# Optimization experiments

Measured on AMD Instinct MI355X. Metric: run time of the kernel, lower is better.

Reference implementation:

```python
import jax, jax.numpy as jnp
import numpy as np

T, B, IN = 64, 4096, 145
H1, H2 = 150, 32


def _lstm_layer(x, w_ih, w_hh, b_ih, b_hh):
    """Single LSTM layer, PyTorch gate order (i, f, g, o).
    x: (T, B, in_dim); w_ih: (4H, in_dim); w_hh: (4H, H); biases: (4H,).
    Returns hidden sequence (T, B, H)."""
    H = w_hh.shape[1]
    Bsz = x.shape[1]
    # Precompute input contribution for all timesteps at once (one big GEMM).
    xg = jnp.einsum('tbi,gi->tbg', x, w_ih) + (b_ih + b_hh)  # (T, B, 4H)
    w_hh_t = w_hh.T  # (H, 4H)

    def step(carry, xg_t):
        h, c = carry
        gates = xg_t + h @ w_hh_t  # (B, 4H)
        i, f, g, o = jnp.split(gates, 4, axis=-1)
        i = jax.nn.sigmoid(i)
        f = jax.nn.sigmoid(f)
        g = jnp.tanh(g)
        o = jax.nn.sigmoid(o)
        c = f * c + i * g
        h = o * jnp.tanh(c)
        return (h, c), h

    h0 = jnp.zeros((Bsz, H), x.dtype)
    c0 = jnp.zeros((Bsz, H), x.dtype)
    _, hs = jax.lax.scan(step, (h0, c0), xg)
    return hs  # (T, B, H)


def _init_lstm_params(key, in_dim, hidden):
    # PyTorch init: U(-k, k) with k = 1/sqrt(hidden)
    k = 1.0 / np.sqrt(hidden)
    ks = jax.random.split(key, 4)
    w_ih = jax.random.uniform(ks[0], (4 * hidden, in_dim), jnp.float32, -k, k)
    w_hh = jax.random.uniform(ks[1], (4 * hidden, hidden), jnp.float32, -k, k)
    b_ih = jax.random.uniform(ks[2], (4 * hidden,), jnp.float32, -k, k)
    b_hh = jax.random.uniform(ks[3], (4 * hidden,), jnp.float32, -k, k)
    return w_ih, w_hh, b_ih, b_hh


def setup_inputs() -> dict:
    key = jax.random.key(0)
    kx, k0, k1, k2 = jax.random.split(key, 4)
    x = jax.random.normal(kx, (T, B, IN), jnp.float32)
    w_ih_l0, w_hh_l0, b_ih_l0, b_hh_l0 = _init_lstm_params(k0, IN, H1)
    w_ih_l1, w_hh_l1, b_ih_l1, b_hh_l1 = _init_lstm_params(k1, H1, H1)
    w_ih_l2, w_hh_l2, b_ih_l2, b_hh_l2 = _init_lstm_params(k2, H1, H2)
    return {
        'x': x,
        'w_ih_l0': w_ih_l0, 'w_hh_l0': w_hh_l0, 'b_ih_l0': b_ih_l0, 'b_hh_l0': b_hh_l0,
        'w_ih_l1': w_ih_l1, 'w_hh_l1': w_hh_l1, 'b_ih_l1': b_ih_l1, 'b_hh_l1': b_hh_l1,
        'w_ih_l2': w_ih_l2, 'w_hh_l2': w_hh_l2, 'b_ih_l2': b_ih_l2, 'b_hh_l2': b_hh_l2,
    }


def reference(x,
              w_ih_l0, w_hh_l0, b_ih_l0, b_hh_l0,
              w_ih_l1, w_hh_l1, b_ih_l1, b_hh_l1,
              w_ih_l2, w_hh_l2, b_ih_l2, b_hh_l2):
    # temporal_model1: 2-layer LSTM (145 -> 150 -> 150)
    h = _lstm_layer(x, w_ih_l0, w_hh_l0, b_ih_l0, b_hh_l0)
    h = _lstm_layer(h, w_ih_l1, w_hh_l1, b_ih_l1, b_hh_l1)
    # temporal_model2: 1-layer LSTM (150 -> 32)
    out2 = _lstm_layer(h, w_ih_l2, w_hh_l2, b_ih_l2, b_hh_l2)
    return out2  # (T, B, 32)
```

## Files before the change

### kernel.cpp

```cpp
#include <hip/hip_runtime.h>


typedef _Float16 f16;
typedef _Float16 f16x8 __attribute__((ext_vector_type(8)));
typedef _Float16 f16x4 __attribute__((ext_vector_type(4)));
typedef float f32x4 __attribute__((ext_vector_type(4)));

#define T_STEPS 64
#define BATCH 4096

__device__ __forceinline__ float fexp(float x) {
  return __builtin_amdgcn_exp2f(x * 1.44269504088896340736f);
}
__device__ __forceinline__ float sigf(float x) {
  return __builtin_amdgcn_rcpf(1.0f + fexp(-x));
}
__device__ __forceinline__ float tanh_f(float x) {
  return 1.0f - 2.0f * __builtin_amdgcn_rcpf(1.0f + fexp(2.0f * x));
}

#define BAR_LGKM() asm volatile("s_waitcnt lgkmcnt(0)\n\ts_barrier" ::: "memory")

__global__ __launch_bounds__(256) void prep_w(
    const float* __restrict__ wih0, const float* __restrict__ bih0, const float* __restrict__ bhh0,
    const float* __restrict__ wih1, const float* __restrict__ bih1, const float* __restrict__ bhh1,
    f16* __restrict__ wprep0, f16* __restrict__ wprep1,
    float* __restrict__ bias0, float* __restrict__ bias1) {
  int idx = blockIdx.x * 256 + threadIdx.x;
  constexpr int WE = 640 * 168;
  if (idx < WE) {
    int c = idx / 168, k = idx - c * 168;
    int gate = c / 160, cg = c - gate * 160;
    float v = (cg < 150 && k < 145) ? wih0[(size_t)(gate * 150 + cg) * 145 + k] : 0.f;
    wprep0[idx] = (f16)v;
  } else if (idx < 2 * WE) {
    int e = idx - WE;
    int c = e / 168, k = e - c * 168;
    int gate = c / 160, cg = c - gate * 160;
    float v = (cg < 150 && k < 150) ? wih1[(size_t)(gate * 150 + cg) * 150 + k] : 0.f;
    wprep1[e] = (f16)v;
  } else if (idx < 2 * WE + 640) {
    int c = idx - 2 * WE;
    int gate = c / 160, cg = c - gate * 160;
    bias0[c] = (cg < 150) ? (bih0[gate * 150 + cg] + bhh0[gate * 150 + cg]) : 0.f;
  } else if (idx < 2 * WE + 1280) {
    int c = idx - 2 * WE - 640;
    int gate = c / 160, cg = c - gate * 160;
    bias1[c] = (cg < 150) ? (bih1[gate * 150 + cg] + bhh1[gate * 150 + cg]) : 0.f;
  }
}

template <int IN_DIM, int SRC_F16>
__global__ __launch_bounds__(512, 4) void gemm_xg4(
    const float* __restrict__ xin_f32, const f16* __restrict__ xin_f16,
    const f16* __restrict__ wprep, const float* __restrict__ bias_pre,
    f16* __restrict__ xg) {
  constexpr int ASTR = 168;
  __shared__ __align__(16) f16 A_lds[128 * ASTR];
  __shared__ __align__(16) f16 W_lds[64 * ASTR];
  __shared__ __align__(16) float bias_lds[640];
  const int tid = threadIdx.x;
  const int mtile = blockIdx.x;
  const int g0 = mtile * 128;

  if constexpr (SRC_F16) {
#pragma unroll
    for (int q = 0; q < 6; ++q) {
      int i = q * 512 + tid;
      if (i < 2688)
        *(f16x8*)(&A_lds[i * 8]) = *(const f16x8*)(xin_f16 + (size_t)g0 * ASTR + (size_t)i * 8);
    }
  } else {
#pragma unroll
    for (int q = 0; q < 10; ++q) {
      int idx = q * 512 + tid;
      int r = idx / 40, c4 = (idx - r * 40) * 4;
      f16x4 o;
      if (c4 + 4 <= IN_DIM) {
        f32x4 v;
        __builtin_memcpy(&v, xin_f32 + (size_t)(g0 + r) * IN_DIM + c4, 16);
#pragma unroll
        for (int j = 0; j < 4; ++j) o[j] = (f16)v[j];
      } else {
#pragma unroll
        for (int j = 0; j < 4; ++j)
          o[j] = (c4 + j < IN_DIM) ? (f16)xin_f32[(size_t)(g0 + r) * IN_DIM + c4 + j] : (f16)0.f;
      }
      *(f16x4*)(&A_lds[r * ASTR + c4]) = o;
    }
  }
  if (tid < 160) *(f32x4*)(&bias_lds[tid * 4]) = *(const f32x4*)(bias_pre + tid * 4);
#pragma unroll
  for (int q = 0; q < 3; ++q) {
    int i = q * 512 + tid;
    if (i < 1344) *(f16x8*)(&W_lds[i * 8]) = *(const f16x8*)(wprep + (size_t)i * 8);
  }
  BAR_LGKM();

  const int l = tid & 63, wv = tid >> 6;
  const int p = wv >> 1, cq = wv & 1;
  const int lrow = l & 15, lk8 = (l >> 4) * 8, r0 = (l >> 4) * 4;
  const int arow0 = (2 * p) * 16 + lrow;
  const int wrow0 = (2 * cq) * 16 + lrow;

  f16x8 pv0, pv1, pv2;
  for (int ch = 0; ch < 10; ++ch) {
    if (ch < 9) {
      const f16* wsrc = wprep + (size_t)(ch + 1) * 10752;
      pv0 = *(const f16x8*)(wsrc + (size_t)tid * 8);
      pv1 = *(const f16x8*)(wsrc + (size_t)(tid + 512) * 8);
      if (tid < 320) pv2 = *(const f16x8*)(wsrc + (size_t)(tid + 1024) * 8);
    }
    const int c0 = ch * 64 + (2 * cq) * 16 + lrow;
    const float bs0 = bias_lds[c0], bs1 = bias_lds[c0 + 16];
    f32x4 a00 = {bs0, bs0, bs0, bs0}, a01 = {bs1, bs1, bs1, bs1};
    f32x4 a10 = a00, a11 = a01;
#pragma unroll
    for (int kc = 0; kc < 5; ++kc) {
      f16x8 a0 = *(const f16x8*)(&A_lds[arow0 * ASTR + kc * 32 + lk8]);
      f16x8 a1 = *(const f16x8*)(&A_lds[(arow0 + 16) * ASTR + kc * 32 + lk8]);
      f16x8 b0 = *(const f16x8*)(&W_lds[wrow0 * ASTR + kc * 32 + lk8]);
      f16x8 b1 = *(const f16x8*)(&W_lds[(wrow0 + 16) * ASTR + kc * 32 + lk8]);
      a00 = __builtin_amdgcn_mfma_f32_16x16x32_f16(a0, b0, a00, 0, 0, 0);
      a01 = __builtin_amdgcn_mfma_f32_16x16x32_f16(a0, b1, a01, 0, 0, 0);
      a10 = __builtin_amdgcn_mfma_f32_16x16x32_f16(a1, b0, a10, 0, 0, 0);
      a11 = __builtin_amdgcn_mfma_f32_16x16x32_f16(a1, b1, a11, 0, 0, 0);
    }
    {
      f16x4 o;
      size_t rg0 = (size_t)(mtile * 8 + 2 * p);
#pragma unroll
      for (int j = 0; j < 4; ++j) o[j] = (f16)a00[j];
      *(f16x4*)(xg + (rg0 * 640 + c0) * 16 + r0) = o;
#pragma unroll
      for (int j = 0; j < 4; ++j) o[j] = (f16)a01[j];
      *(f16x4*)(xg + (rg0 * 640 + c0 + 16) * 16 + r0) = o;
#pragma unroll
      for (int j = 0; j < 4; ++j) o[j] = (f16)a10[j];
      *(f16x4*)(xg + ((rg0 + 1) * 640 + c0) * 16 + r0) = o;
#pragma unroll
      for (int j = 0; j < 4; ++j) o[j] = (f16)a11[j];
      *(f16x4*)(xg + ((rg0 + 1) * 640 + c0 + 16) * 16 + r0) = o;
    }
    if (ch < 9) {
      BAR_LGKM();
      *(f16x8*)(&W_lds[tid * 8]) = pv0;
      *(f16x8*)(&W_lds[(tid + 512) * 8]) = pv1;
      if (tid < 320) *(f16x8*)(&W_lds[(tid + 1024) * 8]) = pv2;
      BAR_LGKM();
    }
  }
}

__global__ __launch_bounds__(640, 2) void lstm_rec(
    const f16* __restrict__ xg, const float* __restrict__ whh,
    f16* __restrict__ hout) {
  constexpr int H = 150, HSTR = 168, CPAD = 640;
  __shared__ __align__(16) f16 hbuf[2][16 * HSTR];
  const int tid = threadIdx.x;
  const int l = tid & 63, w = tid >> 6;
  const int lrow = l & 15, lk8 = (l >> 4) * 8, r0 = (l >> 4) * 4;
  const int col = w * 16 + lrow;
  const int bx = blockIdx.x, b0 = bx * 16;

  for (int i = tid; i < 2 * 16 * HSTR / 8; i += 640) {
    f16x8 z = {};
    *(f16x8*)(&hbuf[0][0] + (size_t)i * 8) = z;
  }

  f16x8 wh[4][5];
#pragma unroll
  for (int g = 0; g < 4; ++g)
#pragma unroll
    for (int kc = 0; kc < 5; ++kc) {
      f16x8 v;
#pragma unroll
      for (int j = 0; j < 8; ++j) {
        int k = kc * 32 + lk8 + j;
        float x = (col < H && k < H) ? whh[((size_t)g * H + col) * H + k] : 0.f;
        v[j] = (f16)x;
      }
      wh[g][kc] = v;
    }
  __syncthreads();

  float creg[4] = {0.f, 0.f, 0.f, 0.f};
  f16x4 pv[4];
#pragma unroll
  for (int g = 0; g < 4; ++g)
    pv[g] = *(const f16x4*)(xg + ((size_t)bx * CPAD + g * 160 + col) * 16 + r0);

  for (int t = 0; t < T_STEPS; ++t) {
    const int cur = t & 1, nxt = cur ^ 1;

    f32x4 acc[4];
#pragma unroll
    for (int g = 0; g < 4; ++g) {
#pragma unroll
      for (int j = 0; j < 4; ++j) acc[g][j] = (float)pv[g][j];
    }
    if (t + 1 < T_STEPS) {
#pragma unroll
      for (int g = 0; g < 4; ++g)
        pv[g] = *(const f16x4*)(xg + ((size_t)((t + 1) * 256 + bx) * CPAD + g * 160 + col) * 16 + r0);
    }
    if (t > 0 && tid < 336) {
      f16x8 v = *(const f16x8*)(&hbuf[cur][tid * 8]);
      *(f16x8*)(hout + ((size_t)(t - 1) * BATCH + b0) * 168 + (size_t)tid * 8) = v;
    }

#pragma unroll
    for (int kc = 0; kc < 5; ++kc) {
      f16x8 a = *(const f16x8*)(&hbuf[cur][lrow * HSTR + kc * 32 + lk8]);
#pragma unroll
      for (int g = 0; g < 4; ++g)
        acc[g] = __builtin_amdgcn_mfma_f32_16x16x32_f16(a, wh[g][kc], acc[g], 0, 0, 0);
    }

#pragma unroll
    for (int j = 0; j < 4; ++j) {
      float iv = sigf(acc[0][j]);
      float fv = sigf(acc[1][j]);
      float gv = tanh_f(acc[2][j]);
      float ov = sigf(acc[3][j]);
      float c = fv * creg[j] + iv * gv;
      creg[j] = c;
      float h = ov * tanh_f(c);
      hbuf[nxt][(r0 + j) * HSTR + col] = (f16)h;
    }

    BAR_LGKM();
  }
  if (tid < 336) {
    f16x8 v = *(const f16x8*)(&hbuf[0][tid * 8]);
    *(f16x8*)(hout + ((size_t)(T_STEPS - 1) * BATCH + b0) * 168 + (size_t)tid * 8) = v;
  }
}

__global__ __launch_bounds__(640, 2) void lstm_rec1f(
    const f16* __restrict__ xg, const float* __restrict__ whh,
    const float* __restrict__ wih2, const float* __restrict__ bih2,
    const float* __restrict__ bhh2, f16* __restrict__ xg2) {
  constexpr int H = 150, HSTR = 168, CPAD = 640;
  __shared__ __align__(16) f16 hbuf[2][16 * HSTR];
  const int tid = threadIdx.x;
  const int l = tid & 63, w = tid >> 6;
  const int lrow = l & 15, lk8 = (l >> 4) * 8, r0 = (l >> 4) * 4;
  const int col = w * 16 + lrow;
  const int bx = blockIdx.x;
  const bool xw = (w < 8);
  const int c2 = w * 16 + lrow;

  for (int i = tid; i < 2 * 16 * HSTR / 8; i += 640) {
    f16x8 z = {};
    *(f16x8*)(&hbuf[0][0] + (size_t)i * 8) = z;
  }

  f16x8 wh[4][5];
#pragma unroll
  for (int g = 0; g < 4; ++g)
#pragma unroll
    for (int kc = 0; kc < 5; ++kc) {
      f16x8 v;
#pragma unroll
      for (int j = 0; j < 8; ++j) {
        int k = kc * 32 + lk8 + j;
        float x = (col < H && k < H) ? whh[((size_t)g * H + col) * H + k] : 0.f;
        v[j] = (f16)x;
      }
      wh[g][kc] = v;
    }
  f16x8 wx2[5];
  float bias2 = 0.f;
  if (xw) {
#pragma unroll
    for (int kc = 0; kc < 5; ++kc) {
      f16x8 v;
#pragma unroll
      for (int j = 0; j < 8; ++j) {
        int k = kc * 32 + lk8 + j;
        float x = (k < 150) ? wih2[(size_t)c2 * 150 + k] : 0.f;
        v[j] = (f16)x;
      }
      wx2[kc] = v;
    }
    bias2 = bih2[c2] + bhh2[c2];
  }
  __syncthreads();

  float creg[4] = {0.f, 0.f, 0.f, 0.f};
  f16x4 pv[4];
#pragma unroll
  for (int g = 0; g < 4; ++g)
    pv[g] = *(const f16x4*)(xg + ((size_t)bx * CPAD + g * 160 + col) * 16 + r0);

  for (int t = 0; t < T_STEPS; ++t) {
    const int cur = t & 1, nxt = cur ^ 1;

    f32x4 acc[4];
#pragma unroll
    for (int g = 0; g < 4; ++g) {
#pragma unroll
      for (int j = 0; j < 4; ++j) acc[g][j] = (float)pv[g][j];
    }
    if (t + 1 < T_STEPS) {
#pragma unroll
      for (int g = 0; g < 4; ++g)
        pv[g] = *(const f16x4*)(xg + ((size_t)((t + 1) * 256 + bx) * CPAD + g * 160 + col) * 16 + r0);
    }

    f32x4 accx = {bias2, bias2, bias2, bias2};
#pragma unroll
    for (int kc = 0; kc < 5; ++kc) {
      f16x8 a = *(const f16x8*)(&hbuf[cur][lrow * HSTR + kc * 32 + lk8]);
#pragma unroll
      for (int g = 0; g < 4; ++g)
        acc[g] = __builtin_amdgcn_mfma_f32_16x16x32_f16(a, wh[g][kc], acc[g], 0, 0, 0);
      if (xw)
        accx = __builtin_amdgcn_mfma_f32_16x16x32_f16(a, wx2[kc], accx, 0, 0, 0);
    }
    if (xw && t > 0) {
      f16x4 o;
#pragma unroll
      for (int j = 0; j < 4; ++j) o[j] = (f16)accx[j];
      *(f16x4*)(xg2 + (((size_t)(t - 1) * 256 + bx) * 128 + c2) * 16 + r0) = o;
    }

#pragma unroll
    for (int j = 0; j < 4; ++j) {
      float iv = sigf(acc[0][j]);
      float fv = sigf(acc[1][j]);
      float gv = tanh_f(acc[2][j]);
      float ov = sigf(acc[3][j]);
      float c = fv * creg[j] + iv * gv;
      creg[j] = c;
      float h = ov * tanh_f(c);
      hbuf[nxt][(r0 + j) * HSTR + col] = (f16)h;
    }

    BAR_LGKM();
  }
  if (xw) {
    f32x4 accx = {bias2, bias2, bias2, bias2};
#pragma unroll
    for (int kc = 0; kc < 5; ++kc) {
      f16x8 a = *(const f16x8*)(&hbuf[0][lrow * HSTR + kc * 32 + lk8]);
      accx = __builtin_amdgcn_mfma_f32_16x16x32_f16(a, wx2[kc], accx, 0, 0, 0);
    }
    f16x4 o;
#pragma unroll
    for (int j = 0; j < 4; ++j) o[j] = (f16)accx[j];
    *(f16x4*)(xg2 + (((size_t)(T_STEPS - 1) * 256 + bx) * 128 + c2) * 16 + r0) = o;
  }
}

__global__ __launch_bounds__(128) void lstm_rec32(
    const f16* __restrict__ xg2, const float* __restrict__ whh2,
    float* __restrict__ yout) {
  constexpr int HSTR2 = 40;
  __shared__ __align__(16) f16 hbuf2[2][16 * HSTR2];
  const int tid = threadIdx.x;
  const int l = tid & 63, w = tid >> 6;
  const int lrow = l & 15, lk8 = (l >> 4) * 8, r0 = (l >> 4) * 4;
  const int cg = w * 16 + lrow;
  const int p = blockIdx.x;
  const int rg = p >> 1, half = p & 1;
  const int b0 = p * 8;
  const bool active = (l < 32);

  for (int i = tid; i < 2 * 16 * HSTR2 / 8; i += 128) {
    f16x8 z = {};
    *(f16x8*)(&hbuf2[0][0] + (size_t)i * 8) = z;
  }

  f16x8 wh2[4];
#pragma unroll
  for (int g = 0; g < 4; ++g) {
    f16x8 v;
#pragma unroll
    for (int j = 0; j < 8; ++j)
      v[j] = (f16)whh2[(size_t)(g * 32 + cg) * 32 + lk8 + j];
    wh2[g] = v;
  }
  __syncthreads();

  float creg[4] = {0.f, 0.f, 0.f, 0.f};
  f16x4 pv[4];
  if (active) {
#pragma unroll
    for (int g = 0; g < 4; ++g)
      pv[g] = *(const f16x4*)(xg2 + ((size_t)rg * 128 + g * 32 + cg) * 16 + half * 8 + r0);
  }

  for (int t = 0; t < T_STEPS; ++t) {
    const int cur = t & 1, nxt = cur ^ 1;

    f32x4 acc[4];
    if (active) {
#pragma unroll
      for (int g = 0; g < 4; ++g) {
#pragma unroll
        for (int j = 0; j < 4; ++j) acc[g][j] = (float)pv[g][j];
      }
      if (t + 1 < T_STEPS) {
#pragma unroll
        for (int g = 0; g < 4; ++g)
          pv[g] = *(const f16x4*)(xg2 + (((size_t)(t + 1) * 256 + rg) * 128 + g * 32 + cg) * 16 + half * 8 + r0);
      }
    } else {
#pragma unroll
      for (int g = 0; g < 4; ++g) acc[g] = f32x4{0.f, 0.f, 0.f, 0.f};
    }

    {
      f16x8 a = *(const f16x8*)(&hbuf2[cur][lrow * HSTR2 + lk8]);
#pragma unroll
      for (int g = 0; g < 4; ++g)
        acc[g] = __builtin_amdgcn_mfma_f32_16x16x32_f16(a, wh2[g], acc[g], 0, 0, 0);
    }

    if (active) {
#pragma unroll
      for (int j = 0; j < 4; ++j) {
        float iv = sigf(acc[0][j]);
        float fv = sigf(acc[1][j]);
        float gv = tanh_f(acc[2][j]);
        float ov = sigf(acc[3][j]);
        float c = fv * creg[j] + iv * gv;
        creg[j] = c;
        float h = ov * tanh_f(c);
        hbuf2[nxt][(r0 + j) * HSTR2 + cg] = (f16)h;
        yout[((size_t)t * BATCH + b0 + r0 + j) * 32 + cg] = h;
      }
    }

    BAR_LGKM();
  }
}

template <int IN_DIM, int H, int MODE>
__global__ __launch_bounds__(512, 2) void lstm_layer(
    const float* __restrict__ xin_f32, const f16* __restrict__ xin_f16,
    const float* __restrict__ w_ih, const float* __restrict__ w_hh,
    const float* __restrict__ b_ih, const float* __restrict__ b_hh,
    f16* __restrict__ hout, float* __restrict__ yout) {
  constexpr int KX = (IN_DIM + 31) / 32;
  constexpr int XSTR = KX * 32 + 8;
  constexpr int KH = (H + 31) / 32;
  constexpr int HSTR = KH * 32 + 8;
  constexpr int NPAD = ((H + 31) / 32) * 32;
  constexpr int NT = NPAD / 32;
  constexpr int GROUPS = NPAD * 4;
  constexpr int UPD_ITERS = (GROUPS + 511) / 512;
  constexpr int XIN_ELEMS = 16 * IN_DIM;
  constexpr int QX = (XIN_ELEMS + 511) / 512;
  constexpr int STG = (16 * XSTR) / 8;
  constexpr int HCP = (16 * HSTR) / 8;
  static_assert(MODE == 0 || XSTR == 168, "");

  __shared__ __align__(16) f16 xbuf[2][16 * XSTR];
  __shared__ __align__(16) f16 hbuf[16 * HSTR];
  __shared__ __align__(16) float gates[NPAD * 84];

  const int tid = threadIdx.x;
  const int l = tid & 63;
  const int wv = tid >> 6;
  const int gate = wv >> 1;
  const int half = wv & 1;
  const int lrow = l & 15;
  const int lk8 = (l >> 4) * 8;
  const int r0 = (l >> 4) * 4;
  const int b0 = blockIdx.x * 16;

  {
    f16* xf = &xbuf[0][0];
    for (int i = tid; i < 2 * 16 * XSTR; i += 512) xf[i] = (f16)0.f;
    for (int i = tid; i < 16 * HSTR; i += 512) hbuf[i] = (f16)0.f;
  }
  const int rbase = half * (NPAD / 2) + lrow;
  float bias_reg[NT];
#pragma unroll
  for (int nt = 0; nt < NT; ++nt) {
    int n = rbase + nt * 16;
    bias_reg[nt] = (n < H) ? (b_ih[gate * H + n] + b_hh[gate * H + n]) : 0.f;
  }
  f16x8 wx[KX][NT], wh[KH][NT];
#pragma unroll
  for (int kc = 0; kc < KX; ++kc)
#pragma unroll
    for (int nt = 0; nt < NT; ++nt) {
      f16x8 wq;
#pragma unroll
      for (int j = 0; j < 8; ++j) {
        int k = kc * 32 + lk8 + j;
        int r = rbase + nt * 16;
        float v = (r < H && k < IN_DIM) ? w_ih[(size_t)(gate * H + r) * IN_DIM + k] : 0.f;
        wq[j] = (f16)v;
      }
      wx[kc][nt] = wq;
    }
#pragma unroll
  for (int kc = 0; kc < KH; ++kc)
#pragma unroll
    for (int nt = 0; nt < NT; ++nt) {
      f16x8 wq;
#pragma unroll
      for (int j = 0; j < 8; ++j) {
        int k = kc * 32 + lk8 + j;
        int r = rbase + nt * 16;
        float v = (r < H && k < H) ? w_hh[(size_t)(gate * H + r) * H + k] : 0.f;
        wq[j] = (f16)v;
      }
      wh[kc][nt] = wq;
    }

  if constexpr (MODE == 0) {
#pragma unroll
    for (int q = 0; q < QX; ++q) {
      int idx = q * 512 + tid;
      if (idx < XIN_ELEMS) {
        float v = xin_f32[(size_t)b0 * IN_DIM + idx];
        int r = idx / IN_DIM, c = idx - r * IN_DIM;
        xbuf[0][r * XSTR + c] = (f16)v;
      }
    }
  } else {
    if (tid < STG) {
      f16x8 v = *(const f16x8*)(xin_f16 + (size_t)b0 * 168 + tid * 8);
      *(f16x8*)(&xbuf[0][tid * 8]) = v;
    }
  }
  __syncthreads();

  float creg[UPD_ITERS][4];
#pragma unroll
  for (int it = 0; it < UPD_ITERS; ++it)
#pragma unroll
    for (int j = 0; j < 4; ++j) creg[it][j] = 0.f;

  float xv[QX];
  f16x8 pv;

  for (int t = 0; t < T_STEPS; ++t) {
    const int cur = t & 1, nxt = cur ^ 1;
    if (t + 1 < T_STEPS) {
      if constexpr (MODE == 0) {
        const float* src = xin_f32 + ((size_t)(t + 1) * BATCH + b0) * IN_DIM;
#pragma unroll
        for (int q = 0; q < QX; ++q) {
          int idx = q * 512 + tid;
          xv[q] = (idx < XIN_ELEMS) ? src[idx] : 0.f;
        }
      } else {
        if (tid < STG)
          pv = *(const f16x8*)(xin_f16 + ((size_t)(t + 1) * BATCH + b0) * 168 + tid * 8);
      }
    }
    if constexpr (MODE != 2) {
      if (t > 0 && tid < HCP) {
        f16x8 v = *(const f16x8*)(&hbuf[tid * 8]);
        *(f16x8*)(hout + ((size_t)(t - 1) * BATCH + b0) * 168 + tid * 8) = v;
      }
    }
    f32x4 acc[NT];
#pragma unroll
    for (int nt = 0; nt < NT; ++nt) {
      float b = bias_reg[nt];
      acc[nt] = f32x4{b, b, b, b};
    }
    {
      const f16* xb = &xbuf[cur][0];
#pragma unroll
      for (int kc = 0; kc < KX; ++kc) {
        f16x8 a = *(const f16x8*)(xb + lrow * XSTR + kc * 32 + lk8);
#pragma unroll
        for (int nt = 0; nt < NT; ++nt)
          acc[nt] = __builtin_amdgcn_mfma_f32_16x16x32_f16(a, wx[kc][nt], acc[nt], 0, 0, 0);
      }
#pragma unroll
      for (int kc = 0; kc < KH; ++kc) {
        f16x8 a = *(const f16x8*)(hbuf + lrow * HSTR + kc * 32 + lk8);
#pragma unroll
        for (int nt = 0; nt < NT; ++nt)
          acc[nt] = __builtin_amdgcn_mfma_f32_16x16x32_f16(a, wh[kc][nt], acc[nt], 0, 0, 0);
      }
    }
#pragma unroll
    for (int nt = 0; nt < NT; ++nt) {
      int n = half * (NPAD / 2) + nt * 16 + lrow;
      *(f32x4*)(&gates[n * 84 + gate * 20 + r0]) = acc[nt];
    }
    BAR_LGKM();
    if (t + 1 < T_STEPS) {
      if constexpr (MODE == 0) {
#pragma unroll
        for (int q = 0; q < QX; ++q) {
          int idx = q * 512 + tid;
          if (idx < XIN_ELEMS) {
            int r = idx / IN_DIM, c = idx - r * IN_DIM;
            xbuf[nxt][r * XSTR + c] = (f16)xv[q];
          }
        }
      } else {
        if (tid < STG) *(f16x8*)(&xbuf[nxt][tid * 8]) = pv;
      }
    }
#pragma unroll
    for (int it = 0; it < UPD_ITERS; ++it) {
      int grp = it * 512 + tid;
      if (grp < GROUPS) {
        int n = grp % NPAD;
        int rb = (grp / NPAD) * 4;
        if (n < H) {
          f32x4 gi = *(const f32x4*)(&gates[n * 84 + 0 + rb]);
          f32x4 gf = *(const f32x4*)(&gates[n * 84 + 20 + rb]);
          f32x4 gg = *(const f32x4*)(&gates[n * 84 + 40 + rb]);
          f32x4 go = *(const f32x4*)(&gates[n * 84 + 60 + rb]);
#pragma unroll
          for (int j = 0; j < 4; ++j) {
            float iv = sigf(gi[j]);
            float fv = sigf(gf[j]);
            float gv = tanh_f(gg[j]);
            float ov = sigf(go[j]);
            float c = fv * creg[it][j] + iv * gv;
            creg[it][j] = c;
            float h = ov * tanh_f(c);
            hbuf[(rb + j) * HSTR + n] = (f16)h;
            if constexpr (MODE == 2) {
              yout[((size_t)t * BATCH + b0 + rb + j) * 32 + n] = h;
            }
          }
        }
      }
    }
    BAR_LGKM();
  }
  if constexpr (MODE != 2) {
    if (tid < HCP) {
      f16x8 v = *(const f16x8*)(&hbuf[tid * 8]);
      *(f16x8*)(hout + ((size_t)(T_STEPS - 1) * BATCH + b0) * 168 + tid * 8) = v;
    }
  }
}

extern "C" void kernel_launch(void* const* d_in, const int* in_sizes, int n_in,
                              void* d_out, int out_size, void* d_ws, size_t ws_size,
                              hipStream_t stream) {
  const float* x = (const float*)d_in[0];
  const float* wih0 = (const float*)d_in[1];
  const float* whh0 = (const float*)d_in[2];
  const float* bih0 = (const float*)d_in[3];
  const float* bhh0 = (const float*)d_in[4];
  const float* wih1 = (const float*)d_in[5];
  const float* whh1 = (const float*)d_in[6];
  const float* bih1 = (const float*)d_in[7];
  const float* bhh1 = (const float*)d_in[8];
  const float* wih2 = (const float*)d_in[9];
  const float* whh2 = (const float*)d_in[10];
  const float* bih2 = (const float*)d_in[11];
  const float* bhh2 = (const float*)d_in[12];

  const size_t HSEQ_BYTES = (size_t)T_STEPS * BATCH * 168 * sizeof(f16);
  const size_t XG_BYTES = (size_t)T_STEPS * BATCH * 640 * sizeof(f16);
  const size_t WPREP_BYTES = (size_t)640 * 168 * sizeof(f16);
  const size_t NEED = HSEQ_BYTES + XG_BYTES + 2 * WPREP_BYTES + 2 * 640 * sizeof(float);
  f16* hws = (f16*)d_ws;
  float* out = (float*)d_out;

  if (ws_size >= NEED) {
    char* base = (char*)d_ws;
    f16* xgbuf = (f16*)(base + HSEQ_BYTES);
    f16* wprep0 = (f16*)(base + HSEQ_BYTES + XG_BYTES);
    f16* wprep1 = (f16*)(base + HSEQ_BYTES + XG_BYTES + WPREP_BYTES);
    float* bias0 = (float*)(base + HSEQ_BYTES + XG_BYTES + 2 * WPREP_BYTES);
    float* bias1 = bias0 + 640;
    f16* xg2buf = hws;

    prep_w<<<dim3(846), dim3(256), 0, stream>>>(wih0, bih0, bhh0, wih1, bih1, bhh1,
                                                wprep0, wprep1, bias0, bias1);
    dim3 gg(2048), gb(512);
    dim3 rg(BATCH / 16), rb(640);
    gemm_xg4<145, 0><<<gg, gb, 0, stream>>>(x, nullptr, wprep0, bias0, xgbuf);
    lstm_rec<<<rg, rb, 0, stream>>>(xgbuf, whh0, hws);
    gemm_xg4<150, 1><<<gg, gb, 0, stream>>>(nullptr, hws, wprep1, bias1, xgbuf);
    lstm_rec1f<<<rg, rb, 0, stream>>>(xgbuf, whh1, wih2, bih2, bhh2, xg2buf);
    lstm_rec32<<<dim3(BATCH / 8), dim3(128), 0, stream>>>(xg2buf, whh2, out);
  } else {
    dim3 grid(BATCH / 16), block(512);
    lstm_layer<145, 150, 0><<<grid, block, 0, stream>>>(x, nullptr, wih0, whh0, bih0, bhh0, hws, nullptr);
    lstm_layer<150, 150, 1><<<grid, block, 0, stream>>>(nullptr, hws, wih1, whh1, bih1, bhh1, hws, nullptr);
    lstm_layer<150, 32, 2><<<grid, block, 0, stream>>>(nullptr, hws, wih2, whh2, bih2, bhh2, nullptr, out);
  }
}
```

Before: 613.7 us.

## Fuse third LSTM layer recurrence into second layer kernel with skewed pipeline

Removes the separate lstm_rec32 kernel by running the 32-wide layer-2 recurrence inside the layer-1 recurrent kernel. Warps 8-9, which were otherwise idle for the input projection, run it two timesteps behind, reading the projected inputs from double-buffered LDS instead of global memory. This drops a kernel launch and the global write and read of xg2, and keeps xg2 in fp32. It adds LDS usage and two extra loop iterations, and lengthens the per-step critical path on warps 8-9. Pointer increments also replace the per-step address recomputation.

```diff
diff --git a/kernel.cpp b/kernel.cpp
--- a/kernel.cpp
+++ b/kernel.cpp
@@ -156,6 +156,8 @@
     const f16* __restrict__ xg, const float* __restrict__ whh,
     f16* __restrict__ hout) {
   constexpr int H = 150, HSTR = 168, CPAD = 640;
+  constexpr size_t XG_TSTRIDE = (size_t)256 * CPAD * 16;
+  constexpr size_t HO_TSTRIDE = (size_t)BATCH * 168;
   __shared__ __align__(16) f16 hbuf[2][16 * HSTR];
   const int tid = threadIdx.x;
   const int l = tid & 63, w = tid >> 6;
@@ -185,10 +187,12 @@
   __syncthreads();
 
   float creg[4] = {0.f, 0.f, 0.f, 0.f};
+  const f16* xgp = xg + ((size_t)bx * CPAD + col) * 16 + r0;
+  f16* houtp = hout + (size_t)b0 * 168 + (size_t)tid * 8;
   f16x4 pv[4];
 #pragma unroll
-  for (int g = 0; g < 4; ++g)
-    pv[g] = *(const f16x4*)(xg + ((size_t)bx * CPAD + g * 160 + col) * 16 + r0);
+  for (int g = 0; g < 4; ++g) pv[g] = *(const f16x4*)(xgp + (size_t)g * 160 * 16);
+  xgp += XG_TSTRIDE;
 
   for (int t = 0; t < T_STEPS; ++t) {
     const int cur = t & 1, nxt = cur ^ 1;
@@ -201,12 +205,13 @@
     }
     if (t + 1 < T_STEPS) {
 #pragma unroll
-      for (int g = 0; g < 4; ++g)
-        pv[g] = *(const f16x4*)(xg + ((size_t)((t + 1) * 256 + bx) * CPAD + g * 160 + col) * 16 + r0);
+      for (int g = 0; g < 4; ++g) pv[g] = *(const f16x4*)(xgp + (size_t)g * 160 * 16);
+      xgp += XG_TSTRIDE;
     }
     if (t > 0 && tid < 336) {
       f16x8 v = *(const f16x8*)(&hbuf[cur][tid * 8]);
-      *(f16x8*)(hout + ((size_t)(t - 1) * BATCH + b0) * 168 + (size_t)tid * 8) = v;
+      *(f16x8*)houtp = v;
+      houtp += HO_TSTRIDE;
     }
 
 #pragma unroll
@@ -233,27 +238,39 @@
   }
   if (tid < 336) {
     f16x8 v = *(const f16x8*)(&hbuf[0][tid * 8]);
-    *(f16x8*)(hout + ((size_t)(T_STEPS - 1) * BATCH + b0) * 168 + (size_t)tid * 8) = v;
-  }
-}
-
-__global__ __launch_bounds__(640, 2) void lstm_rec1f(
+    *(f16x8*)houtp = v;
+  }
+}
+
+__global__ __launch_bounds__(640, 2) void lstm_rec1f2(
     const f16* __restrict__ xg, const float* __restrict__ whh,
     const float* __restrict__ wih2, const float* __restrict__ bih2,
-    const float* __restrict__ bhh2, f16* __restrict__ xg2) {
+    const float* __restrict__ bhh2, const float* __restrict__ whh2,
+    float* __restrict__ yout) {
   constexpr int H = 150, HSTR = 168, CPAD = 640;
+  constexpr int XSTR2 = 20;
+  constexpr int HSTR2 = 40;
+  constexpr size_t XG_TSTRIDE = (size_t)256 * CPAD * 16;
   __shared__ __align__(16) f16 hbuf[2][16 * HSTR];
+  __shared__ __align__(16) float xg2_lds[2][128 * XSTR2];
+  __shared__ __align__(16) f16 h2buf[2][16 * HSTR2];
   const int tid = threadIdx.x;
   const int l = tid & 63, w = tid >> 6;
   const int lrow = l & 15, lk8 = (l >> 4) * 8, r0 = (l >> 4) * 4;
   const int col = w * 16 + lrow;
-  const int bx = blockIdx.x;
+  const int bx = blockIdx.x, b0 = bx * 16;
   const bool xw = (w < 8);
+  const bool l2w = (w >= 8);
   const int c2 = w * 16 + lrow;
+  const int cg2 = (w - 8) * 16 + lrow;
 
   for (int i = tid; i < 2 * 16 * HSTR / 8; i += 640) {
     f16x8 z = {};
     *(f16x8*)(&hbuf[0][0] + (size_t)i * 8) = z;
+  }
+  for (int i = tid; i < 2 * 16 * HSTR2 / 8; i += 640) {
+    f16x8 z = {};
+    *(f16x8*)(&h2buf[0][0] + (size_t)i * 8) = z;
   }
 
   f16x8 wh[4][5];
@@ -286,140 +303,92 @@
     }
     bias2 = bih2[c2] + bhh2[c2];
   }
+  f16x8 wh2[4];
+  if (l2w) {
+#pragma unroll
+    for (int g = 0; g < 4; ++g) {
+      f16x8 v;
+#pragma unroll
+      for (int j = 0; j < 8; ++j)
+        v[j] = (f16)whh2[(size_t)(g * 32 + cg2) * 32 + lk8 + j];
+      wh2[g] = v;
+    }
+  }
   __syncthreads();
 
   float creg[4] = {0.f, 0.f, 0.f, 0.f};
+  float creg2[4] = {0.f, 0.f, 0.f, 0.f};
+  const f16* xgp = xg + ((size_t)bx * CPAD + col) * 16 + r0;
   f16x4 pv[4];
 #pragma unroll
-  for (int g = 0; g < 4; ++g)
-    pv[g] = *(const f16x4*)(xg + ((size_t)bx * CPAD + g * 160 + col) * 16 + r0);
-
-  for (int t = 0; t < T_STEPS; ++t) {
+  for (int g = 0; g < 4; ++g) pv[g] = *(const f16x4*)(xgp + (size_t)g * 160 * 16);
+  xgp += XG_TSTRIDE;
+
+#pragma unroll 1
+  for (int t = 0; t < T_STEPS + 2; ++t) {
     const int cur = t & 1, nxt = cur ^ 1;
 
     f32x4 acc[4];
-#pragma unroll
-    for (int g = 0; g < 4; ++g) {
-#pragma unroll
-      for (int j = 0; j < 4; ++j) acc[g][j] = (float)pv[g][j];
-    }
-    if (t + 1 < T_STEPS) {
+    if (t < T_STEPS) {
+#pragma unroll
+      for (int g = 0; g < 4; ++g) {
+#pragma unroll
+        for (int j = 0; j < 4; ++j) acc[g][j] = (float)pv[g][j];
+      }
+      if (t + 1 < T_STEPS) {
+#pragma unroll
+        for (int g = 0; g < 4; ++g) pv[g] = *(const f16x4*)(xgp + (size_t)g * 160 * 16);
+        xgp += XG_TSTRIDE;
+      }
+    }
+
+    f32x4 accx = {bias2, bias2, bias2, bias2};
+    if (t < T_STEPS) {
+#pragma unroll
+      for (int kc = 0; kc < 5; ++kc) {
+        f16x8 a = *(const f16x8*)(&hbuf[cur][lrow * HSTR + kc * 32 + lk8]);
+#pragma unroll
+        for (int g = 0; g < 4; ++g)
+          acc[g] = __builtin_amdgcn_mfma_f32_16x16x32_f16(a, wh[g][kc], acc[g], 0, 0, 0);
+        if (xw)
+          accx = __builtin_amdgcn_mfma_f32_16x16x32_f16(a, wx2[kc], accx, 0, 0, 0);
+      }
+    } else if (t == T_STEPS && xw) {
+#pragma unroll
+      for (int kc = 0; kc < 5; ++kc) {
+        f16x8 a = *(const f16x8*)(&hbuf[cur][lrow * HSTR + kc * 32 + lk8]);
+        accx = __builtin_amdgcn_mfma_f32_16x16x32_f16(a, wx2[kc], accx, 0, 0, 0);
+      }
+    }
+    if (xw && t >= 1 && t <= T_STEPS) {
+      *(f32x4*)(&xg2_lds[cur][c2 * XSTR2 + r0]) = accx;
+    }
+
+    if (l2w && t >= 2) {
+      const int s = t - 2;
+      f32x4 a2[4];
 #pragma unroll
       for (int g = 0; g < 4; ++g)
-        pv[g] = *(const f16x4*)(xg + ((size_t)((t + 1) * 256 + bx) * CPAD + g * 160 + col) * 16 + r0);
-    }
-
-    f32x4 accx = {bias2, bias2, bias2, bias2};
-#pragma unroll
-    for (int kc = 0; kc < 5; ++kc) {
-      f16x8 a = *(const f16x8*)(&hbuf[cur][lrow * HSTR + kc * 32 + lk8]);
+        a2[g] = *(const f32x4*)(&xg2_lds[nxt][(g * 32 + cg2) * XSTR2 + r0]);
+      f16x8 ah = *(const f16x8*)(&h2buf[nxt][lrow * HSTR2 + lk8]);
 #pragma unroll
       for (int g = 0; g < 4; ++g)
-        acc[g] = __builtin_amdgcn_mfma_f32_16x16x32_f16(a, wh[g][kc], acc[g], 0, 0, 0);
-      if (xw)
-        accx = __builtin_amdgcn_mfma_f32_16x16x32_f16(a, wx2[kc], accx, 0, 0, 0);
-    }
-    if (xw && t > 0) {
-      f16x4 o;
-#pragma unroll
-      for (int j = 0; j < 4; ++j) o[j] = (f16)accx[j];
-      *(f16x4*)(xg2 + (((size_t)(t - 1) * 256 + bx) * 128 + c2) * 16 + r0) = o;
-    }
-
-#pragma unroll
-    for (int j = 0; j < 4; ++j) {
-      float iv = sigf(acc[0][j]);
-      float fv = sigf(acc[1][j]);
-      float gv = tanh_f(acc[2][j]);
-      float ov = sigf(acc[3][j]);
-      float c = fv * creg[j] + iv * gv;
-      creg[j] = c;
-      float h = ov * tanh_f(c);
-      hbuf[nxt][(r0 + j) * HSTR + col] = (f16)h;
-    }
-
-    BAR_LGKM();
-  }
-  if (xw) {
-    f32x4 accx = {bias2, bias2, bias2, bias2};
-#pragma unroll
-    for (int kc = 0; kc < 5; ++kc) {
-      f16x8 a = *(const f16x8*)(&hbuf[0][lrow * HSTR + kc * 32 + lk8]);
-      accx = __builtin_amdgcn_mfma_f32_16x16x32_f16(a, wx2[kc], accx, 0, 0, 0);
-    }
-    f16x4 o;
-#pragma unroll
-    for (int j = 0; j < 4; ++j) o[j] = (f16)accx[j];
-    *(f16x4*)(xg2 + (((size_t)(T_STEPS - 1) * 256 + bx) * 128 + c2) * 16 + r0) = o;
-  }
-}
-
-__global__ __launch_bounds__(128) void lstm_rec32(
-    const f16* __restrict__ xg2, const float* __restrict__ whh2,
-    float* __restrict__ yout) {
-  constexpr int HSTR2 = 40;
-  __shared__ __align__(16) f16 hbuf2[2][16 * HSTR2];
-  const int tid = threadIdx.x;
-  const int l = tid & 63, w = tid >> 6;
-  const int lrow = l & 15, lk8 = (l >> 4) * 8, r0 = (l >> 4) * 4;
-  const int cg = w * 16 + lrow;
-  const int p = blockIdx.x;
-  const int rg = p >> 1, half = p & 1;
-  const int b0 = p * 8;
-  const bool active = (l < 32);
-
-  for (int i = tid; i < 2 * 16 * HSTR2 / 8; i += 128) {
-    f16x8 z = {};
-    *(f16x8*)(&hbuf2[0][0] + (size_t)i * 8) = z;
-  }
-
-  f16x8 wh2[4];
-#pragma unroll
-  for (int g = 0; g < 4; ++g) {
-    f16x8 v;
-#pragma unroll
-    for (int j = 0; j < 8; ++j)
-      v[j] = (f16)whh2[(size_t)(g * 32 + cg) * 32 + lk8 + j];
-    wh2[g] = v;
-  }
-  __syncthreads();
-
-  float creg[4] = {0.f, 0.f, 0.f, 0.f};
-  f16x4 pv[4];
-  if (active) {
-#pragma unroll
-    for (int g = 0; g < 4; ++g)
-      pv[g] = *(const f16x4*)(xg2 + ((size_t)rg * 128 + g * 32 + cg) * 16 + half * 8 + r0);
-  }
-
-  for (int t = 0; t < T_STEPS; ++t) {
-    const int cur = t & 1, nxt = cur ^ 1;
-
-    f32x4 acc[4];
-    if (active) {
-#pragma unroll
-      for (int g = 0; g < 4; ++g) {
-#pragma unroll
-        for (int j = 0; j < 4; ++j) acc[g][j] = (float)pv[g][j];
-      }
-      if (t + 1 < T_STEPS) {
-#pragma unroll
-        for (int g = 0; g < 4; ++g)
-          pv[g] = *(const f16x4*)(xg2 + (((size_t)(t + 1) * 256 + rg) * 128 + g * 32 + cg) * 16 + half * 8 + r0);
-      }
-    } else {
-#pragma unroll
-      for (int g = 0; g < 4; ++g) acc[g] = f32x4{0.f, 0.f, 0.f, 0.f};
-    }
-
-    {
-      f16x8 a = *(const f16x8*)(&hbuf2[cur][lrow * HSTR2 + lk8]);
-#pragma unroll
-      for (int g = 0; g < 4; ++g)
-        acc[g] = __builtin_amdgcn_mfma_f32_16x16x32_f16(a, wh2[g], acc[g], 0, 0, 0);
-    }
-
-    if (active) {
+        a2[g] = __builtin_amdgcn_mfma_f32_16x16x32_f16(ah, wh2[g], a2[g], 0, 0, 0);
+#pragma unroll
+      for (int j = 0; j < 4; ++j) {
+        float iv = sigf(a2[0][j]);
+        float fv = sigf(a2[1][j]);
+        float gv = tanh_f(a2[2][j]);
+        float ov = sigf(a2[3][j]);
+        float c = fv * creg2[j] + iv * gv;
+        creg2[j] = c;
+        float h = ov * tanh_f(c);
+        h2buf[cur][(r0 + j) * HSTR2 + cg2] = (f16)h;
+        yout[((size_t)s * BATCH + b0 + r0 + j) * 32 + cg2] = h;
+      }
+    }
+
+    if (t < T_STEPS) {
 #pragma unroll
       for (int j = 0; j < 4; ++j) {
         float iv = sigf(acc[0][j]);
@@ -429,8 +398,7 @@
         float c = fv * creg[j] + iv * gv;
         creg[j] = c;
         float h = ov * tanh_f(c);
-        hbuf2[nxt][(r0 + j) * HSTR2 + cg] = (f16)h;
-        yout[((size_t)t * BATCH + b0 + r0 + j) * 32 + cg] = h;
+        hbuf[nxt][(r0 + j) * HSTR + col] = (f16)h;
       }
     }
 
@@ -674,7 +642,6 @@
     f16* wprep1 = (f16*)(base + HSEQ_BYTES + XG_BYTES + WPREP_BYTES);
     float* bias0 = (float*)(base + HSEQ_BYTES + XG_BYTES + 2 * WPREP_BYTES);
     float* bias1 = bias0 + 640;
-    f16* xg2buf = hws;
 
     prep_w<<<dim3(846), dim3(256), 0, stream>>>(wih0, bih0, bhh0, wih1, bih1, bhh1,
                                                 wprep0, wprep1, bias0, bias1);
@@ -683,8 +650,7 @@
     gemm_xg4<145, 0><<<gg, gb, 0, stream>>>(x, nullptr, wprep0, bias0, xgbuf);
     lstm_rec<<<rg, rb, 0, stream>>>(xgbuf, whh0, hws);
     gemm_xg4<150, 1><<<gg, gb, 0, stream>>>(nullptr, hws, wprep1, bias1, xgbuf);
-    lstm_rec1f<<<rg, rb, 0, stream>>>(xgbuf, whh1, wih2, bih2, bhh2, xg2buf);
-    lstm_rec32<<<dim3(BATCH / 8), dim3(128), 0, stream>>>(xg2buf, whh2, out);
+    lstm_rec1f2<<<rg, rb, 0, stream>>>(xgbuf, whh1, wih2, bih2, bhh2, whh2, out);
   } else {
     dim3 grid(BATCH / 16), block(512);
     lstm_layer<145, 150, 0><<<grid, block, 0, stream>>>(x, nullptr, wih0, whh0, bih0, bhh0, hws, nullptr);
```

New measurement: 662.9 us. +8.0%, slower.
